# Performance work log

Hardware: AMD Instinct MI355X
Metric: run time of the kernel (lower is better)

## Reference

```python
import jax, jax.numpy as jnp
import numpy as np

CL = 256   # context_length (global in original code)
IL = 64    # inst_length (global in original code)
PC, CH1, CH2, CH3 = 64, 128, 256, 256
CK1, CK2, CK3 = 3, 3, 3
CS1, CS2, CS3 = 1, 2, 2
CP1, CP2, CP3 = 1, 1, 1
BCH1, BCH2, BCH3 = 64, 128, 256
F1, OUT = 1024, 2
B = 2048
C3_OUT = 64 * CH3            # 16384, per __init__ formula with CL-1=255
F1_IN = C3_OUT + BCH3        # 16640


def _conv1d(x, W, b, stride, pad):
    # x: [B, Cin, L], W: [Cout, Cin, K]
    y = jax.lax.conv_general_dilated(x, W, window_strides=(stride,),
                                     padding=[(pad, pad)],
                                     dimension_numbers=("NCH", "OIH", "NCH"))
    return y + b[None, :, None]


def setup_inputs() -> dict:
    key = jax.random.key(0)
    ks = jax.random.split(key, 20)
    s = lambda *sh: 1.0 / np.sqrt(np.prod(sh[1:]))
    def w(k, *sh):
        return jax.random.normal(k, sh, dtype=jnp.float32) * s(*sh)
    return {
        "x": jax.random.normal(ks[0], (B, CL * IL), dtype=jnp.float32),
        "Wp": w(ks[1], PC, IL, 2), "bp": jnp.zeros((PC,), jnp.float32),
        "W1": w(ks[2], CH1, PC, CK1), "b1": jnp.zeros((CH1,), jnp.float32),
        "W2": w(ks[3], CH2, CH1, CK2), "b2": jnp.zeros((CH2,), jnp.float32),
        "W3": w(ks[4], CH3, CH2, CK3), "b3": jnp.zeros((CH3,), jnp.float32),
        "Wb1": w(ks[5], BCH1, IL), "bb1": jnp.zeros((BCH1,), jnp.float32),
        "Wb2": w(ks[6], BCH2, BCH1), "bb2": jnp.zeros((BCH2,), jnp.float32),
        "Wb3": w(ks[7], BCH3, BCH2), "bb3": jnp.zeros((BCH3,), jnp.float32),
        "Wfc1": w(ks[8], F1, F1_IN), "bfc1": jnp.zeros((F1,), jnp.float32),
        "Wfc2": w(ks[9], OUT, F1), "bfc2": jnp.zeros((OUT,), jnp.float32),
    }


def reference(x, Wp, bp, W1, b1, W2, b2, W3, b3,
              Wb1, bb1, Wb2, bb2, Wb3, bb3, Wfc1, bfc1, Wfc2, bfc2):
    xr = x.reshape(-1, CL, IL).transpose(0, 2, 1)   # [B, IL, CL]
    x0 = xr[:, :, 0]                                 # [B, IL]
    # Fused replacement for the convp loop: kernel-2 conv over (x0, x_i)
    # y[:, :, i-1] = Wp[:,:,0] @ x0 + Wp[:,:,1] @ x_i + bp
    y = (jnp.einsum("bi,pi->bp", x0, Wp[:, :, 0])[:, :, None]
         + jnp.einsum("bic,pi->bpc", xr[:, :, 1:], Wp[:, :, 1])
         + bp[None, :, None])                        # [B, PC, CL-1]
    # bypass path on the first instruction (kernel-size-1 convs == matmuls)
    f = jax.nn.relu(x0 @ Wb1.T + bb1)
    f = jax.nn.relu(f @ Wb2.T + bb2)
    f = jax.nn.relu(f @ Wb3.T + bb3)                 # [B, BCH3]
    h = jax.nn.relu(y)
    h = jax.nn.relu(_conv1d(h, W1, b1, CS1, CP1))
    h = jax.nn.relu(_conv1d(h, W2, b2, CS2, CP2))
    h = jax.nn.relu(_conv1d(h, W3, b3, CS3, CP3))    # [B, CH3, 64]
    h = h.reshape(h.shape[0], C3_OUT)
    z = jnp.concatenate([h, f], axis=1)              # [B, F1_IN]
    z = jax.nn.relu(z @ Wfc1.T + bfc1)
    return z @ Wfc2.T + bfc2                         # [B, OUT]
```

## Files before the change

kernel.cpp:

```cpp
#include <hip/hip_runtime.h>
#include <cstdint>
#include <cstddef>

typedef __attribute__((ext_vector_type(8))) short bf16x8;
typedef __attribute__((ext_vector_type(8))) unsigned short ushort8;
typedef __attribute__((ext_vector_type(4))) float f32x4;

__device__ __forceinline__ unsigned short f2bf(float f){
  unsigned int u = __float_as_uint(f);
  unsigned int lsb = (u >> 16) & 1u;
  u += 0x7fffu + lsb;
  return (unsigned short)(u >> 16);
}

__device__ __forceinline__ void gload16(const void* g, void* l){
  __builtin_amdgcn_global_load_lds(
      (const __attribute__((address_space(1))) unsigned int*)g,
      (__attribute__((address_space(3))) unsigned int*)l, 16, 0, 0);
}

__global__ __launch_bounds__(256) void pack_w_bf16_kernel(const float* __restrict__ W,
    unsigned short* __restrict__ Wb, int COUT, int CIN){
  int idx = blockIdx.x*256 + threadIdx.x;
  int tot = COUT*CIN*3;
  if (idx >= tot) return;
  int o = idx/(CIN*3); int r = idx - o*(CIN*3); int kk = r/CIN; int ci = r - kk*CIN;
  Wb[idx] = f2bf(W[(o*CIN + ci)*3 + kk]);
}

__global__ __launch_bounds__(256) void pack_wp_kernel(const float* __restrict__ Wp,
                                                      unsigned short* __restrict__ Bw){
  int idx = blockIdx.x*256 + threadIdx.x;
  if (idx >= 64*128) return;
  int p = idx >> 7, k = idx & 127;
  float v = (k < 64) ? Wp[p*128 + k*2] : Wp[p*128 + (k-64)*2 + 1];
  Bw[idx] = f2bf(v);
}

__global__ __launch_bounds__(256) void f2bf_kernel(const float* __restrict__ src,
                                                   unsigned short* __restrict__ dst, int n){
  int i = blockIdx.x*256 + threadIdx.x;
  if (i < n) dst[i] = f2bf(src[i]);
}

__global__ __launch_bounds__(256) void zero_guards_kernel(unsigned short* __restrict__ buf,
                                                          int LINP, int CIN, int nb){
  int idx = blockIdx.x*256 + threadIdx.x;
  int per = 2*CIN/8;
  if (idx >= nb*per) return;
  int b = idx / per, r = idx - b*per;
  int g = r / (CIN/8), c8 = r - g*(CIN/8);
  ushort8 z = {0,0,0,0,0,0,0,0};
  *(ushort8*)(buf + ((size_t)b*LINP + (size_t)g*(LINP-1))*CIN + c8*8) = z;
}

__global__ __launch_bounds__(256) void branch_kernel(const float* __restrict__ x,
    const float* __restrict__ Wb1, const float* __restrict__ bb1,
    const float* __restrict__ Wb2, const float* __restrict__ bb2,
    const float* __restrict__ Wb3, const float* __restrict__ bb3,
    unsigned short* __restrict__ Hcat){
  __shared__ float s0[64], s1[64], s2[128];
  const int b = blockIdx.x, tid = threadIdx.x;
  const float* xb = x + (size_t)b*16384;
  if (tid < 64) s0[tid] = xb[tid];
  __syncthreads();
  if (tid < 64){
    float a = bb1[tid];
    for (int k=0;k<64;k++) a = fmaf(Wb1[tid*64+k], s0[k], a);
    s1[tid] = fmaxf(a, 0.f);
  }
  __syncthreads();
  if (tid < 128){
    float a = bb2[tid];
    for (int k=0;k<64;k++) a = fmaf(Wb2[tid*64+k], s1[k], a);
    s2[tid] = fmaxf(a, 0.f);
  }
  __syncthreads();
  float a = bb3[tid];
  for (int k=0;k<128;k++) a = fmaf(Wb3[tid*128+k], s2[k], a);
  Hcat[(size_t)b*16640 + 16384 + tid] = f2bf(fmaxf(a, 0.f));
}

__global__ __launch_bounds__(256) void h0_gemm_kernel(const float* __restrict__ x,
    const unsigned short* __restrict__ Bw, const float* __restrict__ bp,
    unsigned short* __restrict__ h0o){
  __shared__ __align__(16) char sAraw[128*256];
  __shared__ __align__(16) char sBraw[64*256];
  const int tid = threadIdx.x;
  const int m0 = blockIdx.x*128;
  #pragma unroll
  for (int i=0;i<16;i++){
    int j = tid + 256*i;
    int row = j >> 5, q = j & 31;
    int m = m0 + row;
    int b = m / 255, c = m - b*255;
    const float* xb = x + (size_t)b*16384;
    int k = q*4;
    const float* src = (k < 64) ? (xb + k) : (xb + (c+1)*64 + (k-64));
    float4 v = *(const float4*)src;
    ushort4 u; u.x=f2bf(v.x); u.y=f2bf(v.y); u.z=f2bf(v.z); u.w=f2bf(v.w);
    *(ushort4*)(sAraw + row*256 + ((k*2) ^ ((row&7)<<4))) = u;
  }
  #pragma unroll
  for (int i=0;i<4;i++){
    int j = tid + 256*i;
    int row = j >> 4, q = j & 15;
    int k = q*8;
    ushort8 u = *(const ushort8*)(Bw + row*128 + k);
    *(ushort8*)(sBraw + row*256 + ((k*2) ^ ((row&7)<<4))) = u;
  }
  __syncthreads();
  const int lane = tid & 63, wid = tid >> 6;
  const int lr = lane & 15, lg = lane >> 4;
  f32x4 acc[2][4];
  #pragma unroll
  for (int a=0;a<2;a++)
    #pragma unroll
    for (int j=0;j<4;j++) acc[a][j] = (f32x4){0,0,0,0};
  #pragma unroll
  for (int ks=0; ks<4; ks++){
    int k = ks*32 + lg*8;
    bf16x8 af[2], bfr[4];
    #pragma unroll
    for (int f=0; f<2; f++){
      int row = wid*32 + f*16 + lr;
      af[f] = *(const bf16x8*)(sAraw + row*256 + ((k*2) ^ ((row&7)<<4)));
    }
    #pragma unroll
    for (int f=0; f<4; f++){
      int row = f*16 + lr;
      bfr[f] = *(const bf16x8*)(sBraw + row*256 + ((k*2) ^ ((row&7)<<4)));
    }
    #pragma unroll
    for (int fi=0; fi<2; fi++)
      #pragma unroll
      for (int fj=0; fj<4; fj++)
        acc[fi][fj] = __builtin_amdgcn_mfma_f32_16x16x32_bf16(af[fi], bfr[fj], acc[fi][fj], 0,0,0);
  }
  #pragma unroll
  for (int fi=0; fi<2; fi++)
    #pragma unroll
    for (int fj=0; fj<4; fj++)
      #pragma unroll
      for (int j=0;j<4;j++){
        int m = m0 + wid*32 + fi*16 + lg*4 + j;
        int n = fj*16 + lr;
        int b = m / 255, t = m - b*255;
        h0o[((size_t)b*257 + t + 1)*64 + n] = f2bf(fmaxf(acc[fi][fj][j] + bp[n], 0.f));
      }
}

template<int CIN,int COUT,int S,int LOUT,int PADIN,int PADOUT,int BM,int MPB,int MF,bool TO_HCAT>
__global__ __launch_bounds__(256) void conv_slab_kernel(
    const unsigned short* __restrict__ in, const unsigned short* __restrict__ Wb,
    const float* __restrict__ bias, unsigned short* __restrict__ out){
  constexpr int NT   = COUT/128;
  constexpr int NCH  = 3*CIN/64;
  constexpr int CP8  = CIN/8;
  constexpr int CB   = CIN*2;
  constexpr int SROWS = 2048/CP8;
  constexpr int LDSROWS = SROWS + 4;
  __shared__ __align__(16) char S_[LDSROWS*CB + 32768];
  char* SA = S_;
  char* SB = S_ + LDSROWS*CB;

  const int tid = threadIdx.x, lane = tid & 63, wv = tid >> 6;
  const int nwg = gridDim.x;
  const int bid = blockIdx.x;
  const int lgid = (bid & 7)*(nwg >> 3) + (bid >> 3);
  const int nt  = lgid % NT;
  const int mtb = lgid / NT;
  const int mt  = mtb % MPB;
  const int b   = mtb / MPB;
  const int n0  = nt*128;
  const int t0  = mt*BM;
  const unsigned short* Ab = in + ((size_t)b*PADIN + (size_t)t0*S)*CIN;

  #pragma unroll
  for (int i=0;i<8;i++){
    int slot = (wv*8+i)*64 + lane;
    int row = slot / CP8, p = slot % CP8;
    gload16(Ab + (size_t)row*CIN + ((p ^ ((row>>1)&7))<<3), SA + (wv*8+i)*1024);
  }
  if (wv == 0 && lane < CP8){
    int row = SROWS, p = lane;
    gload16(Ab + (size_t)row*CIN + ((p ^ ((row>>1)&7))<<3), SA + SROWS*CB);
  }
  if (tid < 3*CP8){
    int r = SROWS + 1 + tid/CP8, p = tid%CP8;
    *(ushort8*)(SA + r*CB + p*16) = (ushort8){0,0,0,0,0,0,0,0};
  }

  const int brow = lane >> 3, bp8 = lane & 7;
  auto stageB = [&](int c, int bufi){
    #pragma unroll
    for (int s=0;s<4;s++){
      int row = wv*32 + s*8 + brow;
      gload16(Wb + (size_t)(n0+row)*(3*CIN) + c*64 + ((bp8 ^ (row&7))<<3),
              SB + bufi*16384 + wv*4096 + s*1024);
    }
  };
  stageB(0, 0);
  __syncthreads();

  const int wm = wv>>1, wn = wv&1;
  const int lr = lane&15, lg = lane>>4;
  f32x4 acc[MF][4];
  #pragma unroll
  for (int i=0;i<MF;i++)
    #pragma unroll
    for (int j=0;j<4;j++) acc[i][j] = (f32x4){0,0,0,0};

  int buf = 0;
  #pragma unroll
  for (int c=0;c<NCH;c++){
    if (c+1 < NCH) stageB(c+1, buf^1);
    const int kk = c/(CIN/64), cc = c%(CIN/64);
    #pragma unroll
    for (int ks=0; ks<2; ks++){
      bf16x8 af[MF], bfr[4];
      #pragma unroll
      for (int f=0;f<MF;f++){
        int row = (wm*(BM/2) + f*16 + lr)*S + kk;
        int ci = cc*8 + ks*4 + lg;
        af[f] = *(const bf16x8*)(SA + row*CB + ((ci ^ ((row>>1)&7))<<4));
      }
      #pragma unroll
      for (int f=0;f<4;f++){
        int rb = wn*64 + f*16 + lr;
        bfr[f] = *(const bf16x8*)(SB + buf*16384 + rb*128 + (((ks*4+lg) ^ (rb&7))<<4));
      }
      #pragma unroll
      for (int fi=0;fi<MF;fi++)
        #pragma unroll
        for (int fj=0;fj<4;fj++)
          acc[fi][fj] = __builtin_amdgcn_mfma_f32_16x16x32_bf16(af[fi], bfr[fj], acc[fi][fj], 0,0,0);
    }
    __syncthreads();
    buf ^= 1;
  }

  #pragma unroll
  for (int fi=0;fi<MF;fi++)
    #pragma unroll
    for (int fj=0;fj<4;fj++)
      #pragma unroll
      for (int j=0;j<4;j++){
        int t = wm*(BM/2) + fi*16 + lg*4 + j;
        int n = n0 + wn*64 + fj*16 + lr;
        if (BM <= LOUT || t < LOUT){
          float v = fmaxf(acc[fi][fj][j] + bias[n], 0.f);
          if (TO_HCAT) out[(size_t)b*16640 + (size_t)n*64 + (t0 + t)] = f2bf(v);
          else         out[((size_t)b*PADOUT + t0 + t + 1)*COUT + n] = f2bf(v);
        }
      }
}

__global__ __launch_bounds__(256) void fc1_gemm_kernel(
    const unsigned short* __restrict__ A, const unsigned short* __restrict__ Bw,
    float* __restrict__ zp, int zoffm, int MT, int KZ){
  __shared__ __align__(16) char sA[128*128];
  __shared__ __align__(16) char sB[128*128];
  const int tid = threadIdx.x;
  const int nwg = gridDim.x;
  const int lgid = (blockIdx.x % 8)*(nwg/8) + blockIdx.x/8;
  const int kz  = lgid / (8*MT);
  const int rem = lgid % (8*MT);
  const int nt  = rem / MT;
  const int mt  = rem % MT;
  const int n0 = nt*128, m0 = mt*128;
  const int lane = tid & 63, wid = tid >> 6;
  const int wm = wid >> 1, wn = wid & 1;
  const int lr = lane & 15, lg = lane >> 4;
  const int srow = lane >> 3;
  const int soff = (((lane&7) ^ srow) << 3);
  f32x4 acc[4][4];
  #pragma unroll
  for (int i=0;i<4;i++)
    #pragma unroll
    for (int j=0;j<4;j++) acc[i][j] = (f32x4){0,0,0,0};
  const int it0 = (kz*260)/KZ, it1 = ((kz+1)*260)/KZ;
  for (int it=it0; it<it1; ++it){
    const size_t k0 = (size_t)it*64;
    __syncthreads();
    #pragma unroll
    for (int s=0;s<4;s++){
      int row = wid*32 + s*8 + srow;
      gload16(A  + (size_t)(m0+row)*16640 + k0 + soff, sA + wid*4096 + s*1024);
      gload16(Bw + (size_t)(n0+row)*16640 + k0 + soff, sB + wid*4096 + s*1024);
    }
    __syncthreads();
    #pragma unroll
    for (int ks=0; ks<2; ks++){
      const int k = ks*32 + lg*8;
      bf16x8 af[4], bfr[4];
      #pragma unroll
      for (int f=0;f<4;f++){
        int rowa = wm*64 + f*16 + lr;
        af[f]  = *(const bf16x8*)(sA + rowa*128 + ((k*2) ^ ((rowa&7)<<4)));
        int rowb = wn*64 + f*16 + lr;
        bfr[f] = *(const bf16x8*)(sB + rowb*128 + ((k*2) ^ ((rowb&7)<<4)));
      }
      #pragma unroll
      for (int fi=0;fi<4;fi++)
        #pragma unroll
        for (int fj=0;fj<4;fj++)
          acc[fi][fj] = __builtin_amdgcn_mfma_f32_16x16x32_bf16(af[fi], bfr[fj], acc[fi][fj], 0,0,0);
    }
  }
  float* zo = zp + (size_t)kz*zoffm;
  #pragma unroll
  for (int fi=0;fi<4;fi++)
    #pragma unroll
    for (int fj=0;fj<4;fj++)
      #pragma unroll
      for (int j=0;j<4;j++){
        int m = m0 + wm*64 + fi*16 + lg*4 + j;
        int n = n0 + wn*64 + fj*16 + lr;
        zo[(size_t)m*1024 + n] = acc[fi][fj][j];
      }
}

__global__ __launch_bounds__(256) void fc2_kernel(const float* __restrict__ zp, int zoffm, int KZ,
    const float* __restrict__ bfc1, const float* __restrict__ Wfc2,
    const float* __restrict__ bfc2, float* __restrict__ out){
  __shared__ float red[4][2];
  const int b = blockIdx.x, tid = threadIdx.x;
  float a0 = 0.f, a1 = 0.f;
  for (int n = tid; n < 1024; n += 256){
    float s = bfc1[n];
    const float* zb = zp + (size_t)b*1024 + n;
    for (int kz = 0; kz < KZ; kz++) s += zb[(size_t)kz*zoffm];
    s = fmaxf(s, 0.f);
    a0 = fmaf(s, Wfc2[n], a0);
    a1 = fmaf(s, Wfc2[1024+n], a1);
  }
  #pragma unroll
  for (int m=32; m>=1; m>>=1){ a0 += __shfl_xor(a0, m, 64); a1 += __shfl_xor(a1, m, 64); }
  const int w = tid >> 6;
  if ((tid & 63) == 0){ red[w][0] = a0; red[w][1] = a1; }
  __syncthreads();
  if (tid == 0){
    out[(size_t)b*2]   = red[0][0]+red[1][0]+red[2][0]+red[3][0] + bfc2[0];
    out[(size_t)b*2+1] = red[0][1]+red[1][1]+red[2][1]+red[3][1] + bfc2[1];
  }
}

extern "C" void kernel_launch(void* const* d_in, const int* in_sizes, int n_in,
                              void* d_out, int out_size, void* d_ws, size_t ws_size,
                              hipStream_t stream){
  const float* x    = (const float*)d_in[0];
  const float* Wp   = (const float*)d_in[1];
  const float* bp   = (const float*)d_in[2];
  const float* W1   = (const float*)d_in[3];
  const float* b1   = (const float*)d_in[4];
  const float* W2   = (const float*)d_in[5];
  const float* b2   = (const float*)d_in[6];
  const float* W3   = (const float*)d_in[7];
  const float* b3   = (const float*)d_in[8];
  const float* Wb1  = (const float*)d_in[9];
  const float* bb1  = (const float*)d_in[10];
  const float* Wb2  = (const float*)d_in[11];
  const float* bb2  = (const float*)d_in[12];
  const float* Wb3  = (const float*)d_in[13];
  const float* bb3  = (const float*)d_in[14];
  const float* Wfc1 = (const float*)d_in[15];
  const float* bfc1 = (const float*)d_in[16];
  const float* Wfc2 = (const float*)d_in[17];
  const float* bfc2 = (const float*)d_in[18];
  float* out = (float*)d_out;

  size_t off = 0;
  char* basep = (char*)d_ws;
  auto carve = [&](size_t bytes)->char*{
    char* q = basep + off; off += (bytes + 255) & ~(size_t)255; return q;
  };
  unsigned short* W1b   = (unsigned short*)carve((size_t)128*3*64*2);
  unsigned short* W2b   = (unsigned short*)carve((size_t)256*3*128*2);
  unsigned short* W3b   = (unsigned short*)carve((size_t)256*3*256*2);
  unsigned short* Bwp   = (unsigned short*)carve((size_t)64*128*2);
  unsigned short* Wfc1b = (unsigned short*)carve((size_t)1024*16640*2);
  size_t fixed = off;

  int Bc = 128, KZ = 64;
  {
    const int bcs[5] = {2048, 1024, 512, 256, 128};
    const int kzs[5] = {4, 8, 16, 32, 64};
    for (int i = 0; i < 5; i++){
      size_t bsz = bcs[i];
      size_t need = fixed + bsz*((size_t)32896+65792+66560+33280) + (size_t)kzs[i]*bsz*4096 + 64*256;
      if (need <= ws_size){ Bc = bcs[i]; KZ = kzs[i]; break; }
    }
  }
  const int NC = 2048/Bc;
  const int MT = Bc/128;
  unsigned short* h0p  = (unsigned short*)carve((size_t)Bc*32896);
  unsigned short* c1p  = (unsigned short*)carve((size_t)Bc*65792);
  unsigned short* c2p  = (unsigned short*)carve((size_t)Bc*66560);
  unsigned short* Hcat = (unsigned short*)carve((size_t)Bc*33280);
  float*          zp   = (float*)carve((size_t)KZ*Bc*4096);
  const int zoffm = Bc*1024;

  hipLaunchKernelGGL(pack_w_bf16_kernel, dim3((128*64*3+255)/256), dim3(256), 0, stream, W1, W1b, 128, 64);
  hipLaunchKernelGGL(pack_w_bf16_kernel, dim3((256*128*3+255)/256), dim3(256), 0, stream, W2, W2b, 256, 128);
  hipLaunchKernelGGL(pack_w_bf16_kernel, dim3((256*256*3+255)/256), dim3(256), 0, stream, W3, W3b, 256, 256);
  hipLaunchKernelGGL(pack_wp_kernel, dim3(32), dim3(256), 0, stream, Wp, Bwp);
  hipLaunchKernelGGL(f2bf_kernel, dim3((17039360+255)/256), dim3(256), 0, stream, Wfc1, Wfc1b, 17039360);

  for (int c = 0; c < NC; ++c){
    const float* xc = x + (size_t)c*Bc*16384;
    hipLaunchKernelGGL(zero_guards_kernel, dim3((Bc*2*64/8+255)/256), dim3(256), 0, stream, h0p, 257, 64, Bc);
    hipLaunchKernelGGL(zero_guards_kernel, dim3((Bc*2*128/8+255)/256), dim3(256), 0, stream, c1p, 257, 128, Bc);
    hipLaunchKernelGGL(zero_guards_kernel, dim3((Bc*2*256/8+255)/256), dim3(256), 0, stream, c2p, 130, 256, Bc);
    hipLaunchKernelGGL(branch_kernel, dim3(Bc), dim3(256), 0, stream,
                       xc, Wb1, bb1, Wb2, bb2, Wb3, bb3, Hcat);
    hipLaunchKernelGGL(h0_gemm_kernel, dim3(Bc*255/128), dim3(256), 0, stream, xc, Bwp, bp, h0p);
    hipLaunchKernelGGL((conv_slab_kernel<64,128,1,255,257,257,256,1,8,false>),
                       dim3(Bc), dim3(256), 0, stream, h0p, W1b, b1, c1p);
    hipLaunchKernelGGL((conv_slab_kernel<128,256,2,128,257,130,64,2,2,false>),
                       dim3(Bc*4), dim3(256), 0, stream, c1p, W2b, b2, c2p);
    hipLaunchKernelGGL((conv_slab_kernel<256,256,2,64,130,0,32,2,1,true>),
                       dim3(Bc*4), dim3(256), 0, stream, c2p, W3b, b3, Hcat);
    hipLaunchKernelGGL(fc1_gemm_kernel, dim3(8*MT*KZ), dim3(256), 0, stream,
                       Hcat, Wfc1b, zp, zoffm, MT, KZ);
    hipLaunchKernelGGL(fc2_kernel, dim3(Bc), dim3(256), 0, stream,
                       zp, zoffm, KZ, bfc1, Wfc2, bfc2, out + (size_t)c*Bc*2);
  }
}
```

Before: 588.8 us.

## Rewrite conv kernels to hold weights in registers with one block per sample

New measurement: 762.4 us. 29.5% more time.

```diff
diff --git a/kernel.cpp b/kernel.cpp
--- a/kernel.cpp
+++ b/kernel.cpp
@@ -150,108 +150,99 @@
       }
 }
 
-template<int CIN,int COUT,int S,int LOUT,int PADIN,int PADOUT,int BM,int MPB,int MF,bool TO_HCAT>
-__global__ __launch_bounds__(256) void conv_slab_kernel(
+template<int CIN,int COUT,int S,int LOUT,int PADIN,int PADOUT,int WM,int WN,int MF,int NF,bool TO_HCAT>
+__global__ __launch_bounds__(512) void conv_breg_kernel(
     const unsigned short* __restrict__ in, const unsigned short* __restrict__ Wb,
     const float* __restrict__ bias, unsigned short* __restrict__ out){
-  constexpr int NT   = COUT/128;
-  constexpr int NCH  = 3*CIN/64;
+  constexpr int K3   = 3*CIN;
+  constexpr int NCH  = K3/64;
   constexpr int CP8  = CIN/8;
   constexpr int CB   = CIN*2;
-  constexpr int SROWS = 2048/CP8;
-  constexpr int LDSROWS = SROWS + 4;
-  __shared__ __align__(16) char S_[LDSROWS*CB + 32768];
-  char* SA = S_;
-  char* SB = S_ + LDSROWS*CB;
+  constexpr int MCOV = WM*MF*16;
+  constexpr int RROWS = (MCOV-1)*S + 3;
+  constexpr int SROWS = (PADIN < RROWS) ? PADIN : RROWS;
+  constexpr int ZROWS = RROWS - SROWS;
+  constexpr int BULK = (SROWS*CP8)/512;
+  constexpr int REM  = SROWS*CP8 - BULK*512;
+  __shared__ __align__(16) char SA[RROWS*CB];
 
   const int tid = threadIdx.x, lane = tid & 63, wv = tid >> 6;
-  const int nwg = gridDim.x;
-  const int bid = blockIdx.x;
-  const int lgid = (bid & 7)*(nwg >> 3) + (bid >> 3);
-  const int nt  = lgid % NT;
-  const int mtb = lgid / NT;
-  const int mt  = mtb % MPB;
-  const int b   = mtb / MPB;
-  const int n0  = nt*128;
-  const int t0  = mt*BM;
-  const unsigned short* Ab = in + ((size_t)b*PADIN + (size_t)t0*S)*CIN;
-
-  #pragma unroll
-  for (int i=0;i<8;i++){
-    int slot = (wv*8+i)*64 + lane;
-    int row = slot / CP8, p = slot % CP8;
-    gload16(Ab + (size_t)row*CIN + ((p ^ ((row>>1)&7))<<3), SA + (wv*8+i)*1024);
-  }
-  if (wv == 0 && lane < CP8){
-    int row = SROWS, p = lane;
-    gload16(Ab + (size_t)row*CIN + ((p ^ ((row>>1)&7))<<3), SA + SROWS*CB);
-  }
-  if (tid < 3*CP8){
-    int r = SROWS + 1 + tid/CP8, p = tid%CP8;
-    *(ushort8*)(SA + r*CB + p*16) = (ushort8){0,0,0,0,0,0,0,0};
-  }
-
-  const int brow = lane >> 3, bp8 = lane & 7;
-  auto stageB = [&](int c, int bufi){
-    #pragma unroll
-    for (int s=0;s<4;s++){
-      int row = wv*32 + s*8 + brow;
-      gload16(Wb + (size_t)(n0+row)*(3*CIN) + c*64 + ((bp8 ^ (row&7))<<3),
-              SB + bufi*16384 + wv*4096 + s*1024);
-    }
+  const int lr = lane & 15, lg = lane >> 4;
+  const int b = blockIdx.x;
+  const int wm = wv / WN, wn = wv % WN;
+  const int mbase = wm*MF*16;
+  const int nbase = wn*NF*16;
+  const unsigned short* Ab = in + (size_t)b*PADIN*CIN;
+  const unsigned short* Wn = Wb + (size_t)nbase*K3;
+
+  #pragma unroll
+  for (int i=0;i<BULK;i++){
+    int slot = i*512 + tid;
+    int row = slot/CP8, p = slot%CP8;
+    gload16(Ab + (size_t)row*CIN + ((p ^ ((row>>(S-1))&7))<<3), SA + i*8192 + wv*1024);
+  }
+  if (REM && tid < REM){
+    int slot = BULK*512 + tid;
+    int row = slot/CP8, p = slot%CP8;
+    gload16(Ab + (size_t)row*CIN + ((p ^ ((row>>(S-1))&7))<<3), SA + BULK*8192);
+  }
+  if (ZROWS && tid < ZROWS*CP8){
+    int row = SROWS + tid/CP8, p = tid%CP8;
+    *(ushort8*)(SA + (size_t)row*CB + p*16) = (ushort8){0,0,0,0,0,0,0,0};
+  }
+
+  bf16x8 breg[3][NF*2];
+  auto loadB = [&](int c, int buf){
+    #pragma unroll
+    for (int fn=0; fn<NF; fn++)
+      #pragma unroll
+      for (int ks=0; ks<2; ks++)
+        breg[buf][fn*2+ks] = *(const bf16x8*)(Wn + (size_t)(fn*16+lr)*K3 + c*64 + ks*32 + lg*8);
   };
-  stageB(0, 0);
-  __syncthreads();
-
-  const int wm = wv>>1, wn = wv&1;
-  const int lr = lane&15, lg = lane>>4;
-  f32x4 acc[MF][4];
+  loadB(0, 0);
+  if (NCH > 1) loadB(1, 1);
+
+  __syncthreads();
+
+  f32x4 acc[MF][NF];
   #pragma unroll
   for (int i=0;i<MF;i++)
     #pragma unroll
-    for (int j=0;j<4;j++) acc[i][j] = (f32x4){0,0,0,0};
-
-  int buf = 0;
-  #pragma unroll
-  for (int c=0;c<NCH;c++){
-    if (c+1 < NCH) stageB(c+1, buf^1);
+    for (int j=0;j<NF;j++) acc[i][j] = (f32x4){0,0,0,0};
+
+  #pragma unroll
+  for (int c=0; c<NCH; c++){
+    if (c+2 < NCH) loadB(c+2, (c+2)%3);
     const int kk = c/(CIN/64), cc = c%(CIN/64);
     #pragma unroll
     for (int ks=0; ks<2; ks++){
-      bf16x8 af[MF], bfr[4];
-      #pragma unroll
-      for (int f=0;f<MF;f++){
-        int row = (wm*(BM/2) + f*16 + lr)*S + kk;
-        int ci = cc*8 + ks*4 + lg;
-        af[f] = *(const bf16x8*)(SA + row*CB + ((ci ^ ((row>>1)&7))<<4));
+      bf16x8 af[MF];
+      #pragma unroll
+      for (int f=0; f<MF; f++){
+        int row = (mbase + f*16 + lr)*S + kk;
+        int slot = cc*8 + ks*4 + lg;
+        af[f] = *(const bf16x8*)(SA + (size_t)row*CB + ((slot ^ ((row>>(S-1))&7))<<4));
       }
       #pragma unroll
-      for (int f=0;f<4;f++){
-        int rb = wn*64 + f*16 + lr;
-        bfr[f] = *(const bf16x8*)(SB + buf*16384 + rb*128 + (((ks*4+lg) ^ (rb&7))<<4));
-      }
-      #pragma unroll
-      for (int fi=0;fi<MF;fi++)
+      for (int fi=0; fi<MF; fi++)
         #pragma unroll
-        for (int fj=0;fj<4;fj++)
-          acc[fi][fj] = __builtin_amdgcn_mfma_f32_16x16x32_bf16(af[fi], bfr[fj], acc[fi][fj], 0,0,0);
-    }
-    __syncthreads();
-    buf ^= 1;
-  }
-
-  #pragma unroll
-  for (int fi=0;fi<MF;fi++)
-    #pragma unroll
-    for (int fj=0;fj<4;fj++)
+        for (int fj=0; fj<NF; fj++)
+          acc[fi][fj] = __builtin_amdgcn_mfma_f32_16x16x32_bf16(af[fi], breg[c%3][fj*2+ks], acc[fi][fj], 0,0,0);
+    }
+  }
+
+  #pragma unroll
+  for (int fi=0; fi<MF; fi++)
+    #pragma unroll
+    for (int fj=0; fj<NF; fj++)
       #pragma unroll
       for (int j=0;j<4;j++){
-        int t = wm*(BM/2) + fi*16 + lg*4 + j;
-        int n = n0 + wn*64 + fj*16 + lr;
-        if (BM <= LOUT || t < LOUT){
+        int t = mbase + fi*16 + lg*4 + j;
+        int n = nbase + fj*16 + lr;
+        if (MCOV <= LOUT || t < LOUT){
           float v = fmaxf(acc[fi][fj][j] + bias[n], 0.f);
-          if (TO_HCAT) out[(size_t)b*16640 + (size_t)n*64 + (t0 + t)] = f2bf(v);
-          else         out[((size_t)b*PADOUT + t0 + t + 1)*COUT + n] = f2bf(v);
+          if (TO_HCAT) out[(size_t)b*16640 + (size_t)n*64 + t] = f2bf(v);
+          else         out[((size_t)b*PADOUT + t + 1)*COUT + n] = f2bf(v);
         }
       }
 }
@@ -415,12 +406,12 @@
     hipLaunchKernelGGL(branch_kernel, dim3(Bc), dim3(256), 0, stream,
                        xc, Wb1, bb1, Wb2, bb2, Wb3, bb3, Hcat);
     hipLaunchKernelGGL(h0_gemm_kernel, dim3(Bc*255/128), dim3(256), 0, stream, xc, Bwp, bp, h0p);
-    hipLaunchKernelGGL((conv_slab_kernel<64,128,1,255,257,257,256,1,8,false>),
-                       dim3(Bc), dim3(256), 0, stream, h0p, W1b, b1, c1p);
-    hipLaunchKernelGGL((conv_slab_kernel<128,256,2,128,257,130,64,2,2,false>),
-                       dim3(Bc*4), dim3(256), 0, stream, c1p, W2b, b2, c2p);
-    hipLaunchKernelGGL((conv_slab_kernel<256,256,2,64,130,0,32,2,1,true>),
-                       dim3(Bc*4), dim3(256), 0, stream, c2p, W3b, b3, Hcat);
+    hipLaunchKernelGGL((conv_breg_kernel<64,128,1,255,257,257,4,2,4,4,false>),
+                       dim3(Bc), dim3(512), 0, stream, h0p, W1b, b1, c1p);
+    hipLaunchKernelGGL((conv_breg_kernel<128,256,2,128,257,130,2,4,4,4,false>),
+                       dim3(Bc), dim3(512), 0, stream, c1p, W2b, b2, c2p);
+    hipLaunchKernelGGL((conv_breg_kernel<256,256,2,64,130,0,2,4,2,4,true>),
+                       dim3(Bc), dim3(512), 0, stream, c2p, W3b, b3, Hcat);
     hipLaunchKernelGGL(fc1_gemm_kernel, dim3(8*MT*KZ), dim3(256), 0, stream,
                        Hcat, Wfc1b, zp, zoffm, MT, KZ);
     hipLaunchKernelGGL(fc2_kernel, dim3(Bc), dim3(256), 0, stream,
```
